# Kernel optimization log

Hardware: AMD Instinct MI355X
Metric: run time of the kernel (lower is better)

The kernel has to match this reference:

```python
import jax, jax.numpy as jnp
import numpy as np

DIM, HEADS, DHEAD = 256, 8, 64
HID = HEADS * DHEAD


def _elu1(x):
    # F.elu(x) + 1 == exp(x) for x<0, x+1 for x>=0
    return jnp.where(x > 0, x + 1.0, jnp.exp(x))


def setup_inputs() -> dict:
    key = jax.random.key(0)
    ks = jax.random.split(key, 6)
    B, H, W = 8, 64, 64
    x = jax.random.normal(ks[0], (B, DIM, H, W), dtype=jnp.float32)
    contact_map = jax.random.uniform(ks[1], (B, 1, H, W), dtype=jnp.float32)
    s_qkv = 1.0 / np.sqrt(DIM)
    Wqkv = jax.random.normal(ks[2], (3 * HID, DIM), dtype=jnp.float32) * s_qkv
    s_out = 1.0 / np.sqrt(HID)
    Wout = jax.random.normal(ks[3], (DIM, HID), dtype=jnp.float32) * s_out
    bout = jax.random.normal(ks[4], (DIM,), dtype=jnp.float32) * 0.01
    contact_scale = jnp.float32(0.1)
    return {"x": x, "contact_map": contact_map, "Wqkv": Wqkv,
            "Wout": Wout, "bout": bout, "contact_scale": contact_scale}


def reference(x, contact_map, Wqkv, Wout, bout, contact_scale):
    b, c, h, w = x.shape
    n = h * w
    xf = x.reshape(b, c, n)                                  # b c n
    qkv = jnp.einsum('oc,bcn->bon', Wqkv, xf)                # b (3*H*D) n
    qkv = qkv.reshape(b, 3, HEADS, DHEAD, n)                 # qkv-major channel order
    q = _elu1(qkv[:, 0])                                     # b h d n
    k = _elu1(qkv[:, 1])
    v = qkv[:, 2]
    cm = contact_map.reshape(b, 1, 1, n)                     # b 1 1 n
    k = k * (1.0 + contact_scale * cm)
    kv = jnp.einsum('bhdn,bhen->bhde', k, v)                 # b h d e
    ksum = k.sum(axis=-1)                                    # b h d
    z = 1.0 / (jnp.einsum('bhdn,bhd->bhn', q, ksum) + 1e-6)  # b h n
    out = jnp.einsum('bhde,bhdn->bhne', kv, q) * z[..., None]  # b h n e
    out = out.transpose(0, 1, 3, 2).reshape(b, HID, n)       # b (h d) n
    y = jnp.einsum('oc,bcn->bon', Wout, out) + bout[None, :, None]
    return y.reshape(b, -1, h, w)
```

## Files before the change

kernel.cpp:

```cpp
#include <hip/hip_runtime.h>
#include <stdint.h>


#define NPIX 4096
#define HIDC 512
#define DIMC 256
#define BATCH 8

typedef __attribute__((ext_vector_type(8))) short bf16x8;
typedef __attribute__((ext_vector_type(4))) float f32x4;
typedef __attribute__((ext_vector_type(16))) float f32x16;

__device__ __forceinline__ float bf2f(unsigned short h) {
    unsigned int u = ((unsigned int)h) << 16; float f;
    __builtin_memcpy(&f, &u, 4); return f;
}
__device__ __forceinline__ unsigned short f2bf(float f) {
    unsigned int u; __builtin_memcpy(&u, &f, 4);
    u += 0x7fffu + ((u >> 16) & 1u);
    return (unsigned short)(u >> 16);
}
__device__ __forceinline__ float elu1(float x) {
    return x > 0.f ? x + 1.f : __expf(x);
}
__device__ __forceinline__ void gl16(const unsigned short* g, unsigned short* l) {
    __builtin_amdgcn_global_load_lds(
        (__attribute__((address_space(1))) const void*)g,
        (__attribute__((address_space(3))) void*)l, 16, 0, 0);
}

__global__ __launch_bounds__(256) void k_convW(
    const float* __restrict__ Wqkv, const float* __restrict__ Wout,
    unsigned short* __restrict__ Wb, unsigned short* __restrict__ Wob)
{
    int i4 = (blockIdx.x * 256 + threadIdx.x) * 4;
    const int NW1 = 1536 * 256;
    float4 v; unsigned short* dst;
    if (i4 < NW1) { v = *(const float4*)&Wqkv[i4]; dst = Wb + i4; }
    else { int j = i4 - NW1; v = *(const float4*)&Wout[j]; dst = Wob + j; }
    ushort4 o; o.x = f2bf(v.x); o.y = f2bf(v.y); o.z = f2bf(v.z); o.w = f2bf(v.w);
    *(ushort4*)dst = o;
}

__global__ __launch_bounds__(256) void k_tx(
    const float* __restrict__ x, unsigned short* __restrict__ xT)
{
    __shared__ float tile[32][33];
    const int n0 = blockIdx.x * 32, c0 = blockIdx.y * 32, b = blockIdx.z;
    const int t = threadIdx.x;
    const int r = t >> 3, c4 = (t & 7) * 4;
    float4 v = *(const float4*)&x[((size_t)b * DIMC + c0 + r) * NPIX + n0 + c4];
    tile[r][c4 + 0] = v.x; tile[r][c4 + 1] = v.y;
    tile[r][c4 + 2] = v.z; tile[r][c4 + 3] = v.w;
    __syncthreads();
    ushort4 o;
    unsigned short* op = (unsigned short*)&o;
#pragma unroll
    for (int i = 0; i < 4; i++) op[i] = f2bf(tile[c4 + i][r]);
    *(ushort4*)&xT[((size_t)b * NPIX + n0 + r) * DIMC + c0 + c4] = o;
}


#define CHALF(ACC, KH, BUF, SWAP)                                              \
    _Pragma("unroll")                                                          \
    for (int ks = 0; ks < 8; ks++) {                                           \
        bf16x8 wf = *(const bf16x8*)&Ws[BUF][(wn * 32 + l31) * 128 +           \
                            (((ks * 2 + lhi) ^ (l31 & 7)) * 8)];               \
        if (SWAP)                                                              \
            ACC = __builtin_amdgcn_mfma_f32_32x32x16_bf16(wf, af[(KH) * 8 + ks], ACC, 0, 0, 0); \
        else                                                                   \
            ACC = __builtin_amdgcn_mfma_f32_32x32x16_bf16(af[(KH) * 8 + ks], wf, ACC, 0, 0, 0); \
    }

__global__ __launch_bounds__(256, 2) void k_fused(
    const unsigned short* __restrict__ xT,
    const unsigned short* __restrict__ Wb,
    const float* __restrict__ cmp,
    const float* __restrict__ csp,
    unsigned short* __restrict__ qT,
    float* __restrict__ kvp,
    float* __restrict__ ksump)
{
    const int b  = blockIdx.y;
    const int m0 = blockIdx.x * 64;
    const int t  = threadIdx.x;
    const int wave = t >> 6, lane = t & 63;
    const int wm = wave >> 1, wn = wave & 1;
    const int l31 = lane & 31, lhi = lane >> 5;

    __shared__ unsigned short Ws[2][64 * 128];
    __shared__ unsigned short kS[64 * 64];
    __shared__ unsigned short vS[64 * 64];

    const float cs = *csp;

    auto stageW = [&](int R, int kh, int buf) {
#pragma unroll
        for (int i = 0; i < 4; i++) {
            const int rowbase = wave * 16 + i * 4;
            const int row = rowbase + (lane >> 4);
            gl16(&Wb[(size_t)(R + row) * DIMC + kh * 128 +
                     (((lane & 15) ^ (row & 7)) * 8)],
                 &Ws[buf][rowbase * 128]);
        }
    };

    stageW(0, 0, 0);

    bf16x8 af[16];
    {
        const unsigned short* Ab = xT + ((size_t)b * NPIX + m0 + wm * 32 + l31) * DIMC;
#pragma unroll
        for (int ks = 0; ks < 16; ks++)
            af[ks] = *(const bf16x8*)&Ab[ks * 16 + lhi * 8];
    }
    const float gv = 1.f + cs * cmp[(size_t)b * NPIX + m0 + wm * 32 + l31];

    for (int nt = 0; nt < 8; nt++) {
        __syncthreads();
        stageW(nt * 64, 1, 1);
        f32x16 acc;
#pragma unroll
        for (int r = 0; r < 16; r++) acc[r] = 0.f;
        CHALF(acc, 0, 0, 0)
        __syncthreads();
        stageW(nt < 7 ? (nt + 1) * 64 : 512, 0, 0);
        CHALF(acc, 1, 1, 0)
        unsigned short* qg = qT + ((size_t)b * NPIX + m0 + wm * 32) * HIDC
                           + nt * 64 + wn * 32 + l31;
#pragma unroll
        for (int r = 0; r < 16; r++) {
            const int rp = (r & 3) + 8 * (r >> 2) + 4 * lhi;
            qg[(size_t)rp * HIDC] = f2bf(elu1(acc[r]));
        }
    }

    for (int h = 0; h < 8; h++) {
        __syncthreads();
        stageW(512 + h * 64, 1, 1);
        if (h > 0) {
            f32x16 kvacc;
#pragma unroll
            for (int r = 0; r < 16; r++) kvacc[r] = 0.f;
#pragma unroll
            for (int pk = 0; pk < 4; pk++) {
                const int co = ((pk * 2 + lhi) ^ (l31 & 7)) * 8;
                bf16x8 kf = *(const bf16x8*)&kS[(wm * 32 + l31) * 64 + co];
                bf16x8 vf = *(const bf16x8*)&vS[(wn * 32 + l31) * 64 + co];
                kvacc = __builtin_amdgcn_mfma_f32_32x32x16_bf16(kf, vf, kvacc, 0, 0, 0);
            }
            float* kvb = kvp + (size_t)(b * 8 + (h - 1)) * 4096;
#pragma unroll
            for (int r = 0; r < 16; r++) {
                const int d = wm * 32 + (r & 3) + 8 * (r >> 2) + 4 * lhi;
                atomicAdd(&kvb[d * 64 + wn * 32 + l31], kvacc[r]);
            }
        }
        f32x16 acc;
#pragma unroll
        for (int r = 0; r < 16; r++) acc[r] = 0.f;
        CHALF(acc, 0, 0, 1)
        __syncthreads();
        stageW(1024 + h * 64, 0, 0);
        CHALF(acc, 1, 1, 1)
#pragma unroll
        for (int r = 0; r < 16; r++) {
            const int ch = wn * 32 + (r & 3) + 8 * (r >> 2) + 4 * lhi;
            const int pixl = wm * 32 + l31;
            kS[ch * 64 + (pixl ^ ((ch & 7) << 3))] = f2bf(elu1(acc[r]) * gv);
        }

        __syncthreads();
        stageW(1024 + h * 64, 1, 1);
        {
            const int ch = t & 63, part = t >> 6;
            float s = 0.f;
#pragma unroll
            for (int j2 = 0; j2 < 2; j2++) {
                const int j = part * 2 + j2;
                const bf16x8 kr = *(const bf16x8*)&kS[ch * 64 + ((j ^ (ch & 7)) * 8)];
#pragma unroll
                for (int u = 0; u < 8; u++) s += bf2f(((const unsigned short*)&kr)[u]);
            }
            atomicAdd(&ksump[(size_t)(b * 8 + h) * 64 + ch], s);
        }
        f32x16 acc2;
#pragma unroll
        for (int r = 0; r < 16; r++) acc2[r] = 0.f;
        CHALF(acc2, 0, 0, 1)
        __syncthreads();
        if (h < 7) stageW(512 + (h + 1) * 64, 0, 0);
        CHALF(acc2, 1, 1, 1)
#pragma unroll
        for (int r = 0; r < 16; r++) {
            const int ch = wn * 32 + (r & 3) + 8 * (r >> 2) + 4 * lhi;
            const int pixl = wm * 32 + l31;
            vS[ch * 64 + (pixl ^ ((ch & 7) << 3))] = f2bf(acc2[r]);
        }
    }

    __syncthreads();
    {
        f32x16 kvacc;
#pragma unroll
        for (int r = 0; r < 16; r++) kvacc[r] = 0.f;
#pragma unroll
        for (int pk = 0; pk < 4; pk++) {
            const int co = ((pk * 2 + lhi) ^ (l31 & 7)) * 8;
            bf16x8 kf = *(const bf16x8*)&kS[(wm * 32 + l31) * 64 + co];
            bf16x8 vf = *(const bf16x8*)&vS[(wn * 32 + l31) * 64 + co];
            kvacc = __builtin_amdgcn_mfma_f32_32x32x16_bf16(kf, vf, kvacc, 0, 0, 0);
        }
        float* kvb = kvp + (size_t)(b * 8 + 7) * 4096;
#pragma unroll
        for (int r = 0; r < 16; r++) {
            const int d = wm * 32 + (r & 3) + 8 * (r >> 2) + 4 * lhi;
            atomicAdd(&kvb[d * 64 + wn * 32 + l31], kvacc[r]);
        }
    }
}

#define LS3 72
__global__ __launch_bounds__(256) void k_out(
    const unsigned short* __restrict__ qT,
    const float* __restrict__ kv, const float* __restrict__ ksum,
    unsigned short* __restrict__ outT)
{
    const int bh = blockIdx.y, p0 = blockIdx.x * 128;
    const int b = bh >> 3, h = bh & 7;
    const int t = threadIdx.x, wave = t >> 6, lane = t & 63;
    const int l31 = lane & 31, lhi = lane >> 5;

    __shared__ unsigned short Aq[128 * LS3];
    __shared__ unsigned short Bv[96 * LS3];

    const unsigned short* qg = qT + ((size_t)b * NPIX + p0) * HIDC + h * 64;
#pragma unroll
    for (int i = 0; i < 4; i++) {
        int idx = t + i * 256;
        int row = idx >> 3, c8 = (idx & 7) * 8;
        *(uint4*)&Aq[row * LS3 + c8] = *(const uint4*)&qg[(size_t)row * HIDC + c8];
    }
    const float* kvg = kv + (size_t)bh * 4096;
#pragma unroll
    for (int i = 0; i < 16; i++) {
        int idx = t + i * 256;
        int d = idx >> 6, e = idx & 63;
        Bv[e * LS3 + d] = f2bf(kvg[idx]);
    }
    if (t < 64) {
        float ksv = ksum[bh * 64 + t];
        unsigned short hi = f2bf(ksv);
        Bv[64 * LS3 + t] = hi;
        Bv[65 * LS3 + t] = f2bf(ksv - bf2f(hi));
    }
    for (int i = t; i < 30 * 64; i += 256)
        Bv[(66 + (i >> 6)) * LS3 + (i & 63)] = 0;
    __syncthreads();

    f32x16 acc[3];
#pragma unroll
    for (int j = 0; j < 3; j++)
#pragma unroll
        for (int r = 0; r < 16; r++) acc[j][r] = 0.f;

#pragma unroll
    for (int ksub = 0; ksub < 4; ksub++) {
        const int koff = ksub * 16 + lhi * 8;
        bf16x8 af = *(const bf16x8*)&Aq[(wave * 32 + l31) * LS3 + koff];
#pragma unroll
        for (int nf = 0; nf < 3; nf++) {
            bf16x8 bfg = *(const bf16x8*)&Bv[(nf * 32 + l31) * LS3 + koff];
            acc[nf] = __builtin_amdgcn_mfma_f32_32x32x16_bf16(af, bfg, acc[nf], 0, 0, 0);
        }
    }

    unsigned short* og = outT + ((size_t)b * NPIX + p0 + wave * 32) * HIDC + h * 64;
#pragma unroll
    for (int r = 0; r < 16; r++) {
        float hi = __shfl(acc[2][r], lane & 32);
        float lo = __shfl(acc[2][r], (lane & 32) | 1);
        float z = 1.f / (hi + lo + 1e-6f);
        int prow = (r & 3) + 8 * (r >> 2) + 4 * lhi;
#pragma unroll
        for (int nf = 0; nf < 2; nf++)
            og[(size_t)prow * HIDC + nf * 32 + l31] = f2bf(acc[nf][r] * z);
    }
}

__global__ __launch_bounds__(256) void k_y(
    const unsigned short* __restrict__ outT,
    const unsigned short* __restrict__ Wob,
    const float* __restrict__ bout,
    float* __restrict__ y)
{
    const int b  = blockIdx.z;
    const int m0 = blockIdx.x * 128;
    const int n0 = blockIdx.y * 128;
    const int t = threadIdx.x;
    const int wave = t >> 6, lane = t & 63;
    const int wm = wave >> 1, wn = wave & 1;
    const int lrow = lane & 15, quad = lane >> 4;

    __shared__ unsigned short As[128 * 64];
    __shared__ unsigned short Bs[128 * 64];

    const unsigned short* Ag = outT + ((size_t)b * NPIX + m0) * HIDC;
    const unsigned short* Bg = Wob + (size_t)n0 * HIDC;

    f32x4 acc[4][4];
#pragma unroll
    for (int i = 0; i < 4; i++)
#pragma unroll
        for (int j = 0; j < 4; j++) acc[i][j] = (f32x4){0.f, 0.f, 0.f, 0.f};

    const int r8  = lane >> 3;
    const int jg8 = (((lane & 7) ^ r8) & 7) * 8;
    const int xswA = (lrow & 7);

    for (int k0 = 0; k0 < HIDC; k0 += 64) {
#pragma unroll
        for (int i = 0; i < 4; i++) {
            const int rowg = wave * 32 + i * 8;
            gl16(&Ag[(size_t)(rowg + r8) * HIDC + k0 + jg8], &As[rowg * 64]);
            gl16(&Bg[(size_t)(rowg + r8) * HIDC + k0 + jg8], &Bs[rowg * 64]);
        }
        __syncthreads();
#pragma unroll
        for (int ksb = 0; ksb < 2; ksb++) {
            bf16x8 af[4], bfr[4];
#pragma unroll
            for (int mt = 0; mt < 4; mt++) {
                const int row = wm * 64 + mt * 16 + lrow;
                af[mt] = *(const bf16x8*)&As[row * 64 + (((ksb * 4 + quad) ^ xswA)) * 8];
            }
#pragma unroll
            for (int nt = 0; nt < 4; nt++) {
                const int row = wn * 64 + nt * 16 + lrow;
                bfr[nt] = *(const bf16x8*)&Bs[row * 64 + (((ksb * 4 + quad) ^ xswA)) * 8];
            }
#pragma unroll
            for (int mt = 0; mt < 4; mt++)
#pragma unroll
                for (int nt = 0; nt < 4; nt++)
                    acc[mt][nt] = __builtin_amdgcn_mfma_f32_16x16x32_bf16(
                        af[mt], bfr[nt], acc[mt][nt], 0, 0, 0);
        }
        __syncthreads();
    }

#pragma unroll
    for (int mt = 0; mt < 4; mt++) {
        const int pixel0 = m0 + wm * 64 + mt * 16 + quad * 4;
#pragma unroll
        for (int nt = 0; nt < 4; nt++) {
            const int o = n0 + wn * 64 + nt * 16 + lrow;
            const float bias = bout[o];
            f32x4 a = acc[mt][nt];
            float4 st; st.x = a[0] + bias; st.y = a[1] + bias;
            st.z = a[2] + bias; st.w = a[3] + bias;
            *(float4*)&y[((size_t)b * DIMC + o) * NPIX + pixel0] = st;
        }
    }
}

extern "C" void kernel_launch(void* const* d_in, const int* in_sizes, int n_in,
                              void* d_out, int out_size, void* d_ws, size_t ws_size,
                              hipStream_t stream) {
    (void)in_sizes; (void)n_in; (void)out_size; (void)ws_size;
    const float* x    = (const float*)d_in[0];
    const float* cm   = (const float*)d_in[1];
    const float* Wqkv = (const float*)d_in[2];
    const float* Wout = (const float*)d_in[3];
    const float* bout = (const float*)d_in[4];
    const float* csp  = (const float*)d_in[5];
    float* y = (float*)d_out;

    const size_t qn = (size_t)BATCH * HIDC * NPIX;
    char* ws = (char*)d_ws;
    unsigned short* qT   = (unsigned short*)ws;                 ws += qn * 2;
    unsigned short* outT = (unsigned short*)ws;                 ws += qn * 2;
    unsigned short* xT   = outT;
    float* kvp   = (float*)ws;                                  ws += (size_t)64 * 64 * 64 * 4;
    float* ksump = (float*)ws;                                  ws += (size_t)64 * 64 * 4;
    unsigned short* Wb  = (unsigned short*)ws;                  ws += (size_t)1536 * 256 * 2;
    unsigned short* Wob = (unsigned short*)ws;

    hipMemsetAsync(kvp, 0, ((size_t)64 * 64 * 64 + 64 * 64) * sizeof(float), stream);
    k_convW<<<512, 256, 0, stream>>>(Wqkv, Wout, Wb, Wob);
    k_tx   <<<dim3(128, 8, 8), 256, 0, stream>>>(x, xT);
    k_fused<<<dim3(64, 8),     256, 0, stream>>>(xT, Wb, cm, csp, qT, kvp, ksump);
    k_out  <<<dim3(32, 64),    256, 0, stream>>>(qT, kvp, ksump, outT);
    k_y    <<<dim3(32, 2, 8),  256, 0, stream>>>(outT, Wob, bout, y);
}
```

Before: 235.8 us.

## Widen fused QKV block to 128 pixels and read weights directly from global

The fused QKV/kv kernel now runs 512-thread blocks covering 128 pixels each, halving the block count. Weight tiles are no longer staged through double-buffered LDS with async copies; each lane loads its weight fragments straight from global memory (L2), which removes most of the barriers. The kv outer product now contracts over 128 pixels per block, which halves the atomic traffic. Waves 0-3 compute kv while waves 4-7 compute ksum in parallel. The tradeoff is exposed global-load latency in front of every MFMA and fewer blocks to fill the CUs.

```diff
diff --git a/kernel.cpp b/kernel.cpp
--- a/kernel.cpp
+++ b/kernel.cpp
@@ -61,18 +61,7 @@
 }
 
 
-#define CHALF(ACC, KH, BUF, SWAP)                                              \
-    _Pragma("unroll")                                                          \
-    for (int ks = 0; ks < 8; ks++) {                                           \
-        bf16x8 wf = *(const bf16x8*)&Ws[BUF][(wn * 32 + l31) * 128 +           \
-                            (((ks * 2 + lhi) ^ (l31 & 7)) * 8)];               \
-        if (SWAP)                                                              \
-            ACC = __builtin_amdgcn_mfma_f32_32x32x16_bf16(wf, af[(KH) * 8 + ks], ACC, 0, 0, 0); \
-        else                                                                   \
-            ACC = __builtin_amdgcn_mfma_f32_32x32x16_bf16(af[(KH) * 8 + ks], wf, ACC, 0, 0, 0); \
-    }
-
-__global__ __launch_bounds__(256, 2) void k_fused(
+__global__ __launch_bounds__(512, 2) void k_fused(
     const unsigned short* __restrict__ xT,
     const unsigned short* __restrict__ Wb,
     const float* __restrict__ cmp,
@@ -82,30 +71,16 @@
     float* __restrict__ ksump)
 {
     const int b  = blockIdx.y;
-    const int m0 = blockIdx.x * 64;
+    const int m0 = blockIdx.x * 128;
     const int t  = threadIdx.x;
     const int wave = t >> 6, lane = t & 63;
     const int wm = wave >> 1, wn = wave & 1;
     const int l31 = lane & 31, lhi = lane >> 5;
 
-    __shared__ unsigned short Ws[2][64 * 128];
-    __shared__ unsigned short kS[64 * 64];
-    __shared__ unsigned short vS[64 * 64];
+    __shared__ unsigned short kS[64 * 128];
+    __shared__ unsigned short vS[64 * 128];
 
     const float cs = *csp;
-
-    auto stageW = [&](int R, int kh, int buf) {
-#pragma unroll
-        for (int i = 0; i < 4; i++) {
-            const int rowbase = wave * 16 + i * 4;
-            const int row = rowbase + (lane >> 4);
-            gl16(&Wb[(size_t)(R + row) * DIMC + kh * 128 +
-                     (((lane & 15) ^ (row & 7)) * 8)],
-                 &Ws[buf][rowbase * 128]);
-        }
-    };
-
-    stageW(0, 0, 0);
 
     bf16x8 af[16];
     {
@@ -116,16 +91,17 @@
     }
     const float gv = 1.f + cs * cmp[(size_t)b * NPIX + m0 + wm * 32 + l31];
 
+#pragma unroll
     for (int nt = 0; nt < 8; nt++) {
-        __syncthreads();
-        stageW(nt * 64, 1, 1);
+        const unsigned short* Wr = Wb + (size_t)(nt * 64 + wn * 32 + l31) * DIMC + lhi * 8;
         f32x16 acc;
 #pragma unroll
         for (int r = 0; r < 16; r++) acc[r] = 0.f;
-        CHALF(acc, 0, 0, 0)
-        __syncthreads();
-        stageW(nt < 7 ? (nt + 1) * 64 : 512, 0, 0);
-        CHALF(acc, 1, 1, 0)
+#pragma unroll
+        for (int ks = 0; ks < 16; ks++) {
+            bf16x8 wf = *(const bf16x8*)&Wr[ks * 16];
+            acc = __builtin_amdgcn_mfma_f32_32x32x16_bf16(af[ks], wf, acc, 0, 0, 0);
+        }
         unsigned short* qg = qT + ((size_t)b * NPIX + m0 + wm * 32) * HIDC
                            + nt * 64 + wn * 32 + l31;
 #pragma unroll
@@ -135,87 +111,72 @@
         }
     }
 
+#pragma unroll 1
     for (int h = 0; h < 8; h++) {
+        const unsigned short* Wk = Wb + (size_t)(512 + h * 64 + wn * 32 + l31) * DIMC + lhi * 8;
+        f32x16 acc;
+#pragma unroll
+        for (int r = 0; r < 16; r++) acc[r] = 0.f;
+#pragma unroll
+        for (int ks = 0; ks < 16; ks++) {
+            bf16x8 wf = *(const bf16x8*)&Wk[ks * 16];
+            acc = __builtin_amdgcn_mfma_f32_32x32x16_bf16(wf, af[ks], acc, 0, 0, 0);
+        }
         __syncthreads();
-        stageW(512 + h * 64, 1, 1);
-        if (h > 0) {
-            f32x16 kvacc;
-#pragma unroll
-            for (int r = 0; r < 16; r++) kvacc[r] = 0.f;
-#pragma unroll
-            for (int pk = 0; pk < 4; pk++) {
-                const int co = ((pk * 2 + lhi) ^ (l31 & 7)) * 8;
-                bf16x8 kf = *(const bf16x8*)&kS[(wm * 32 + l31) * 64 + co];
-                bf16x8 vf = *(const bf16x8*)&vS[(wn * 32 + l31) * 64 + co];
-                kvacc = __builtin_amdgcn_mfma_f32_32x32x16_bf16(kf, vf, kvacc, 0, 0, 0);
-            }
-            float* kvb = kvp + (size_t)(b * 8 + (h - 1)) * 4096;
-#pragma unroll
-            for (int r = 0; r < 16; r++) {
-                const int d = wm * 32 + (r & 3) + 8 * (r >> 2) + 4 * lhi;
-                atomicAdd(&kvb[d * 64 + wn * 32 + l31], kvacc[r]);
-            }
-        }
-        f32x16 acc;
-#pragma unroll
-        for (int r = 0; r < 16; r++) acc[r] = 0.f;
-        CHALF(acc, 0, 0, 1)
-        __syncthreads();
-        stageW(1024 + h * 64, 0, 0);
-        CHALF(acc, 1, 1, 1)
 #pragma unroll
         for (int r = 0; r < 16; r++) {
             const int ch = wn * 32 + (r & 3) + 8 * (r >> 2) + 4 * lhi;
-            const int pixl = wm * 32 + l31;
-            kS[ch * 64 + (pixl ^ ((ch & 7) << 3))] = f2bf(elu1(acc[r]) * gv);
-        }
-
-        __syncthreads();
-        stageW(1024 + h * 64, 1, 1);
-        {
-            const int ch = t & 63, part = t >> 6;
-            float s = 0.f;
-#pragma unroll
-            for (int j2 = 0; j2 < 2; j2++) {
-                const int j = part * 2 + j2;
-                const bf16x8 kr = *(const bf16x8*)&kS[ch * 64 + ((j ^ (ch & 7)) * 8)];
-#pragma unroll
-                for (int u = 0; u < 8; u++) s += bf2f(((const unsigned short*)&kr)[u]);
-            }
-            atomicAdd(&ksump[(size_t)(b * 8 + h) * 64 + ch], s);
-        }
+            const int pix = wm * 32 + l31;
+            kS[ch * 128 + (pix ^ ((ch & 7) << 3))] = f2bf(elu1(acc[r]) * gv);
+        }
+
+        const unsigned short* Wv = Wb + (size_t)(1024 + h * 64 + wn * 32 + l31) * DIMC + lhi * 8;
         f32x16 acc2;
 #pragma unroll
         for (int r = 0; r < 16; r++) acc2[r] = 0.f;
-        CHALF(acc2, 0, 0, 1)
-        __syncthreads();
-        if (h < 7) stageW(512 + (h + 1) * 64, 0, 0);
-        CHALF(acc2, 1, 1, 1)
+#pragma unroll
+        for (int ks = 0; ks < 16; ks++) {
+            bf16x8 wf = *(const bf16x8*)&Wv[ks * 16];
+            acc2 = __builtin_amdgcn_mfma_f32_32x32x16_bf16(wf, af[ks], acc2, 0, 0, 0);
+        }
 #pragma unroll
         for (int r = 0; r < 16; r++) {
             const int ch = wn * 32 + (r & 3) + 8 * (r >> 2) + 4 * lhi;
-            const int pixl = wm * 32 + l31;
-            vS[ch * 64 + (pixl ^ ((ch & 7) << 3))] = f2bf(acc2[r]);
-        }
-    }
-
-    __syncthreads();
-    {
-        f32x16 kvacc;
-#pragma unroll
-        for (int r = 0; r < 16; r++) kvacc[r] = 0.f;
-#pragma unroll
-        for (int pk = 0; pk < 4; pk++) {
-            const int co = ((pk * 2 + lhi) ^ (l31 & 7)) * 8;
-            bf16x8 kf = *(const bf16x8*)&kS[(wm * 32 + l31) * 64 + co];
-            bf16x8 vf = *(const bf16x8*)&vS[(wn * 32 + l31) * 64 + co];
-            kvacc = __builtin_amdgcn_mfma_f32_32x32x16_bf16(kf, vf, kvacc, 0, 0, 0);
-        }
-        float* kvb = kvp + (size_t)(b * 8 + 7) * 4096;
-#pragma unroll
-        for (int r = 0; r < 16; r++) {
-            const int d = wm * 32 + (r & 3) + 8 * (r >> 2) + 4 * lhi;
-            atomicAdd(&kvb[d * 64 + wn * 32 + l31], kvacc[r]);
+            const int pix = wm * 32 + l31;
+            vS[ch * 128 + (pix ^ ((ch & 7) << 3))] = f2bf(acc2[r]);
+        }
+        __syncthreads();
+
+        if (wave < 4) {
+            const int wmk = wave >> 1, wnk = wave & 1;
+            f32x16 kvacc;
+#pragma unroll
+            for (int r = 0; r < 16; r++) kvacc[r] = 0.f;
+#pragma unroll
+            for (int pk = 0; pk < 8; pk++) {
+                const int co = ((pk * 2 + lhi) ^ (l31 & 7)) * 8;
+                bf16x8 kf = *(const bf16x8*)&kS[(wmk * 32 + l31) * 128 + co];
+                bf16x8 vf = *(const bf16x8*)&vS[(wnk * 32 + l31) * 128 + co];
+                kvacc = __builtin_amdgcn_mfma_f32_32x32x16_bf16(kf, vf, kvacc, 0, 0, 0);
+            }
+            float* kvb = kvp + (size_t)(b * 8 + h) * 4096;
+#pragma unroll
+            for (int r = 0; r < 16; r++) {
+                const int d = wmk * 32 + (r & 3) + 8 * (r >> 2) + 4 * lhi;
+                atomicAdd(&kvb[d * 64 + wnk * 32 + l31], kvacc[r]);
+            }
+        } else {
+            const int t2 = t & 255;
+            const int ch = t2 & 63, part = t2 >> 6;
+            float s = 0.f;
+#pragma unroll
+            for (int j2 = 0; j2 < 4; j2++) {
+                const int j = part * 4 + j2;
+                const bf16x8 kr = *(const bf16x8*)&kS[ch * 128 + ((j ^ (ch & 7)) * 8)];
+#pragma unroll
+                for (int u = 0; u < 8; u++) s += bf2f(((const unsigned short*)&kr)[u]);
+            }
+            atomicAdd(&ksump[(size_t)(b * 8 + h) * 64 + ch], s);
         }
     }
 }
@@ -389,7 +350,7 @@
     hipMemsetAsync(kvp, 0, ((size_t)64 * 64 * 64 + 64 * 64) * sizeof(float), stream);
     k_convW<<<512, 256, 0, stream>>>(Wqkv, Wout, Wb, Wob);
     k_tx   <<<dim3(128, 8, 8), 256, 0, stream>>>(x, xT);
-    k_fused<<<dim3(64, 8),     256, 0, stream>>>(xT, Wb, cm, csp, qT, kvp, ksump);
+    k_fused<<<dim3(32, 8),     512, 0, stream>>>(xT, Wb, cm, csp, qT, kvp, ksump);
     k_out  <<<dim3(32, 64),    256, 0, stream>>>(qT, kvp, ksump, outT);
     k_y    <<<dim3(32, 2, 8),  256, 0, stream>>>(outT, Wob, bout, y);
 }
```

New measurement: 252.1 us. +6.9%, slower.
